# Kernel optimization log

Measured on AMD Instinct MI355X. Metric: run time of the kernel, lower is better.

The kernel has to match this reference:

```python
import jax, jax.numpy as jnp
import numpy as np

EMBED_DIM = 2048
NUM_Q_HEADS = 16
NUM_KV_HEADS = 4
HEAD_DIM = EMBED_DIM // NUM_Q_HEADS  # 128
N_REP = NUM_Q_HEADS // NUM_KV_HEADS  # 4


def setup_inputs() -> dict:
    key = jax.random.key(0)
    ks = jax.random.split(key, 8)
    B, T, C = 2, 2048, EMBED_DIM
    s = 0.02
    return {
        "x": jax.random.normal(ks[0], (B, T, C), dtype=jnp.float32),
        "Wq": jax.random.normal(ks[1], (C, NUM_Q_HEADS * HEAD_DIM), dtype=jnp.float32) * s,
        "bq": jax.random.normal(ks[2], (NUM_Q_HEADS * HEAD_DIM,), dtype=jnp.float32) * s,
        "Wk": jax.random.normal(ks[3], (C, NUM_KV_HEADS * HEAD_DIM), dtype=jnp.float32) * s,
        "bk": jax.random.normal(ks[4], (NUM_KV_HEADS * HEAD_DIM,), dtype=jnp.float32) * s,
        "Wv": jax.random.normal(ks[5], (C, NUM_KV_HEADS * HEAD_DIM), dtype=jnp.float32) * s,
        "bv": jax.random.normal(ks[6], (NUM_KV_HEADS * HEAD_DIM,), dtype=jnp.float32) * s,
        "Wo": jax.random.normal(ks[7], (C, C), dtype=jnp.float32) * s,
    }


def reference(x, Wq, bq, Wk, bk, Wv, bv, Wo):
    B, T, C = x.shape
    # Projections (torch Linear with bias; weights stored as [in, out])
    q = (x @ Wq + bq).reshape(B, T, NUM_KV_HEADS, N_REP, HEAD_DIM)
    k = (x @ Wk + bk).reshape(B, T, NUM_KV_HEADS, HEAD_DIM)
    v = (x @ Wv + bv).reshape(B, T, NUM_KV_HEADS, HEAD_DIM)
    # GQA: group query heads per kv head instead of materializing repeated K/V.
    # q: [B, G, n_rep, Tq, d], k/v: [B, G, Tk, d]
    q = q.transpose(0, 2, 3, 1, 4)  # B, G, n_rep, T, d
    k = k.transpose(0, 2, 1, 3)     # B, G, T, d
    v = v.transpose(0, 2, 1, 3)
    scale = 1.0 / jnp.sqrt(jnp.asarray(HEAD_DIM, dtype=x.dtype))
    scores = jnp.einsum('bgnqd,bgkd->bgnqk', q, k) * scale
    attn = jax.nn.softmax(scores, axis=-1)
    out = jnp.einsum('bgnqk,bgkd->bgnqd', attn, v)  # B, G, n_rep, T, d
    # merge heads back: (G, n_rep) -> Hq, then [B, T, C]
    out = out.transpose(0, 3, 1, 2, 4).reshape(B, T, C)
    return out @ Wo
```

## Files before the change

kernel.cpp:

```cpp
#include <hip/hip_runtime.h>
#include <hip/hip_bf16.h>
#include <cstdint>
#include <cstddef>

typedef __bf16 bf16;
typedef __attribute__((ext_vector_type(8))) __bf16 bf16x8;
typedef __attribute__((ext_vector_type(4))) float f32x4;
typedef __attribute__((ext_vector_type(16))) float f32x16;

#define KPAD 136

__device__ __forceinline__ void async16(const void* g, void* l) {
  __builtin_amdgcn_global_load_lds(
      (const __attribute__((address_space(1))) void*)g,
      (__attribute__((address_space(3))) void*)l,
      16, 0, 0);
}

__global__ void cvt_x(const float* __restrict__ in, bf16* __restrict__ out, int n8) {
  int i = blockIdx.x * 256 + threadIdx.x;
  if (i >= n8) return;
  const float* src = in + (size_t)i * 8;
  float4 f0 = *reinterpret_cast<const float4*>(src);
  float4 f1 = *reinterpret_cast<const float4*>(src + 4);
  bf16x8 v = {(bf16)f0.x, (bf16)f0.y, (bf16)f0.z, (bf16)f0.w,
              (bf16)f1.x, (bf16)f1.y, (bf16)f1.z, (bf16)f1.w};
  *reinterpret_cast<bf16x8*>(out + (size_t)i * 8) = v;
}

template <typename CT, bool HAS_BIAS>
__global__ __launch_bounds__(256, 2)
void gemm_bt(const bf16* __restrict__ A, const bf16* __restrict__ Bt,
             const bf16* __restrict__ bias, CT* __restrict__ C,
             int M, int N, int K) {
  __shared__ bf16 smem[4][128 * 64];
  const int tid = threadIdx.x;
  const int wave = tid >> 6, lane = tid & 63;
  const int quad = lane >> 4, l15 = lane & 15;
  const int row0 = blockIdx.y * 128;
  const int col0 = blockIdx.x * 128;
  const int wm = wave & 1, wn = wave >> 1;
  const int sw = l15 & 7;

  const f32x4 fz = {0.f, 0.f, 0.f, 0.f};
  f32x4 acc[4][4];
#pragma unroll
  for (int i = 0; i < 4; ++i)
#pragma unroll
    for (int j = 0; j < 4; ++j) acc[i][j] = fz;

#define STAGE(buf, k0)                                                         \
  {                                                                            \
    _Pragma("unroll")                                                          \
    for (int j = 0; j < 4; ++j) {                                              \
      int c = tid + j * 256;                                                   \
      int r = c >> 3;                                                          \
      int gs = (c & 7) ^ (r & 7);                                              \
      async16(A + (size_t)(row0 + r) * K + (k0) + gs * 8, &smem[(buf)*2][c * 8]);   \
      async16(Bt + (size_t)(col0 + r) * K + (k0) + gs * 8, &smem[(buf)*2 + 1][c * 8]); \
    }                                                                          \
  }

  STAGE(0, 0);
  __syncthreads();

  const int nt = K >> 6;
  for (int t = 0; t < nt; ++t) {
    const int cur = t & 1;
    if (t + 1 < nt) STAGE(cur ^ 1, (t + 1) << 6);

    const bf16* As = smem[cur * 2];
    const bf16* Bs = smem[cur * 2 + 1];
    bf16x8 a[4][2], b[4][2];
#pragma unroll
    for (int mf = 0; mf < 4; ++mf) {
      int ra = wm * 64 + mf * 16 + l15;
      int rb = wn * 64 + mf * 16 + l15;
#pragma unroll
      for (int ks = 0; ks < 2; ++ks) {
        int pg = (ks * 4 + quad) ^ sw;
        a[mf][ks] = *reinterpret_cast<const bf16x8*>(&As[ra * 64 + pg * 8]);
        b[mf][ks] = *reinterpret_cast<const bf16x8*>(&Bs[rb * 64 + pg * 8]);
      }
    }
#pragma unroll
    for (int ks = 0; ks < 2; ++ks)
#pragma unroll
      for (int mf = 0; mf < 4; ++mf)
#pragma unroll
        for (int nf = 0; nf < 4; ++nf)
          acc[mf][nf] = __builtin_amdgcn_mfma_f32_16x16x32_bf16(a[mf][ks], b[nf][ks],
                                                                acc[mf][nf], 0, 0, 0);

    __syncthreads();
  }
#undef STAGE

#pragma unroll
  for (int i = 0; i < 4; ++i) {
    int m = row0 + wm * 64 + i * 16 + quad * 4;
#pragma unroll
    for (int j = 0; j < 4; ++j) {
      int n = col0 + wn * 64 + j * 16 + l15;
      float bv = HAS_BIAS ? (float)bias[n] : 0.f;
#pragma unroll
      for (int r = 0; r < 4; ++r)
        C[(size_t)(m + r) * N + n] = (CT)(acc[i][j][r] + bv);
    }
  }
}

__global__ void transpose2d_cvt(const float* __restrict__ in, bf16* __restrict__ out,
                                int R, int C) {
  __shared__ float t[32][33];
  const int tx = threadIdx.x & 31, ty = threadIdx.x >> 5;
  const int c0 = blockIdx.x * 32, r0 = blockIdx.y * 32;
#pragma unroll
  for (int i = 0; i < 4; ++i)
    t[ty + i * 8][tx] = in[(size_t)(r0 + ty + i * 8) * C + c0 + tx];
  __syncthreads();
#pragma unroll
  for (int i = 0; i < 4; ++i)
    out[(size_t)(c0 + ty + i * 8) * R + r0 + tx] = (bf16)t[tx][ty + i * 8];
}

__global__ void transpose_v(const bf16* __restrict__ QKV, bf16* __restrict__ Vt) {
  const int z = blockIdx.z;
  const int b = z >> 2, g = z & 3;
  const bf16* in = QKV + (size_t)b * 2048 * 3072 + 2560 + g * 128;
  bf16* out = Vt + (size_t)z * 128 * 2048;
  __shared__ bf16 t[32][33];
  const int tx = threadIdx.x & 31, ty = threadIdx.x >> 5;
  const int d0 = blockIdx.x * 32;
  const int t0 = blockIdx.y * 32;
#pragma unroll
  for (int i = 0; i < 4; ++i)
    t[ty + i * 8][tx] = in[(size_t)(t0 + ty + i * 8) * 3072 + d0 + tx];
  __syncthreads();
#pragma unroll
  for (int i = 0; i < 4; ++i)
    out[(size_t)(d0 + ty + i * 8) * 2048 + t0 + tx] = t[tx][ty + i * 8];
}

__global__ void concat_bias(const float* __restrict__ bq, const float* __restrict__ bk,
                            const float* __restrict__ bv, bf16* __restrict__ out) {
  int i = blockIdx.x * 256 + threadIdx.x;
  float v;
  if (i < 2048) v = bq[i];
  else if (i < 2560) v = bk[i - 2048];
  else v = bv[i - 2560];
  out[i] = (bf16)v;
}

__global__ __launch_bounds__(256, 2)
void attn_kernel(const bf16* __restrict__ QKV, const bf16* __restrict__ Vt,
                 bf16* __restrict__ Out) {
  const int bid = blockIdx.x;
  const int qt = bid & 15;
  const int bh = bid >> 4;
  const int b = bh >> 4, h = bh & 15, g = h >> 2;
  const int tid = threadIdx.x;
  const int wave = tid >> 6, lane = tid & 63;
  const int l31 = lane & 31, half = lane >> 5;

  __shared__ bf16 smem[32768];
  bf16* Qstage = smem;

  const bf16* Qbase = QKV + ((size_t)b * 2048 + qt * 128) * 3072 + h * 128;
#pragma unroll
  for (int j = 0; j < 8; ++j) {
    int c = tid + j * 256;
    *reinterpret_cast<bf16x8*>(&Qstage[(c >> 4) * KPAD + (c & 15) * 8]) =
        *reinterpret_cast<const bf16x8*>(Qbase + (size_t)(c >> 4) * 3072 + (c & 15) * 8);
  }
  __syncthreads();
  bf16x8 qf[8];
#pragma unroll
  for (int ks = 0; ks < 8; ++ks)
    qf[ks] = *reinterpret_cast<const bf16x8*>(
        &Qstage[(wave * 32 + l31) * KPAD + ks * 16 + half * 8]);
  __syncthreads();

  const bf16* Kbase = QKV + (size_t)b * 2048 * 3072 + 2048 + g * 128;
  const bf16* Vbase = Vt + (size_t)(b * 4 + g) * 128 * 2048;

#define ATTN_STAGE(buf, t0_)                                                  \
  {                                                                           \
    bf16* KsD = smem + (buf)*16384;                                           \
    bf16* VsD = smem + (buf)*16384 + 8192;                                    \
    _Pragma("unroll")                                                         \
    for (int j = 0; j < 4; ++j) {                                             \
      int c = tid + j * 256;                                                  \
      int rk = c >> 4, gk = (c & 15) ^ (rk & 15);                             \
      async16(Kbase + (size_t)((t0_) + rk) * 3072 + gk * 8, &KsD[c * 8]);     \
      int rv = c >> 3, gv = (c & 7) ^ (rv & 7);                               \
      async16(Vbase + (size_t)rv * 2048 + (t0_) + gv * 8, &VsD[c * 8]);       \
    }                                                                         \
  }

  ATTN_STAGE(0, 0);
  __syncthreads();

  f32x16 po[4];
#pragma unroll
  for (int j = 0; j < 4; ++j)
#pragma unroll
    for (int r = 0; r < 16; ++r) po[j][r] = 0.f;
  float lsum = 0.f;
  const float sc2 = 0.12751746030545063f;

  for (int t = 0; t < 32; ++t) {
    const int cur = t & 1;
    if (t + 1 < 32) ATTN_STAGE(cur ^ 1, (t + 1) * 64);

    const bf16* KsB = smem + cur * 16384;
    const bf16* VsB = smem + cur * 16384 + 8192;

    f32x16 s[2];
#pragma unroll
    for (int nt = 0; nt < 2; ++nt)
#pragma unroll
      for (int r = 0; r < 16; ++r) s[nt][r] = 0.f;
#pragma unroll
    for (int ks = 0; ks < 8; ++ks) {
#pragma unroll
      for (int nt = 0; nt < 2; ++nt) {
        bf16x8 kf = *reinterpret_cast<const bf16x8*>(
            &KsB[(nt * 32 + l31) * 128 + (((ks * 2 + half) ^ (l31 & 15))) * 8]);
        s[nt] = __builtin_amdgcn_mfma_f32_32x32x16_bf16(kf, qf[ks], s[nt], 0, 0, 0);
      }
    }

#pragma unroll
    for (int nt = 0; nt < 2; ++nt)
#pragma unroll
      for (int r = 0; r < 16; ++r) {
        float p = exp2f(s[nt][r] * sc2);
        lsum += p;
        s[nt][r] = p;
      }

#pragma unroll
    for (int ks2 = 0; ks2 < 4; ++ks2) {
      const int nt = ks2 >> 1;
      const int a = (ks2 & 1) * 8;
      uint32_t x0, x1, x2, x3;
      asm("v_cvt_pk_bf16_f32 %0, %1, %2" : "=v"(x0) : "v"(s[nt][a + 0]), "v"(s[nt][a + 1]));
      asm("v_cvt_pk_bf16_f32 %0, %1, %2" : "=v"(x1) : "v"(s[nt][a + 2]), "v"(s[nt][a + 3]));
      asm("v_cvt_pk_bf16_f32 %0, %1, %2" : "=v"(x2) : "v"(s[nt][a + 4]), "v"(s[nt][a + 5]));
      asm("v_cvt_pk_bf16_f32 %0, %1, %2" : "=v"(x3) : "v"(s[nt][a + 6]), "v"(s[nt][a + 7]));
      asm("v_permlane32_swap_b32 %0, %1" : "+v"(x0), "+v"(x2));
      asm("v_permlane32_swap_b32 %0, %1" : "+v"(x1), "+v"(x3));
      union { uint32_t u[4]; bf16x8 v; } pu;
      pu.u[0] = x0; pu.u[1] = x1; pu.u[2] = x2; pu.u[3] = x3;
      const bf16x8 pf = pu.v;
#pragma unroll
      for (int nd = 0; nd < 4; ++nd) {
        bf16x8 vf = *reinterpret_cast<const bf16x8*>(
            &VsB[(nd * 32 + l31) * 64 + (((ks2 * 2 + half) ^ (l31 & 7))) * 8]);
        po[nd] = __builtin_amdgcn_mfma_f32_32x32x16_bf16(pf, vf, po[nd], 0, 0, 0);
      }
    }

    __syncthreads();
  }
#undef ATTN_STAGE

  float l = lsum + __shfl_xor(lsum, 32, 64);
  float inv = 1.0f / l;

  const size_t qrow0 = (size_t)b * 2048 + (size_t)qt * 128 + wave * 32;
#pragma unroll
  for (int r = 0; r < 16; ++r) {
    int row = (r & 3) + 8 * (r >> 2) + 4 * half;
    float invr = __shfl(inv, row, 64);
#pragma unroll
    for (int nt = 0; nt < 4; ++nt)
      Out[(qrow0 + row) * 2048 + h * 128 + nt * 32 + l31] = (bf16)(po[nt][r] * invr);
  }
}

extern "C" void kernel_launch(void* const* d_in, const int* in_sizes, int n_in,
                              void* d_out, int out_size, void* d_ws, size_t ws_size,
                              hipStream_t stream) {
  const float* x  = (const float*)d_in[0];
  const float* Wq = (const float*)d_in[1];
  const float* bq = (const float*)d_in[2];
  const float* Wk = (const float*)d_in[3];
  const float* bk = (const float*)d_in[4];
  const float* Wv = (const float*)d_in[5];
  const float* bv = (const float*)d_in[6];
  const float* Wo = (const float*)d_in[7];
  float* out = (float*)d_out;
  bf16* ws = (bf16*)d_ws;

  bf16* wqkvT = ws;
  bf16* biasq = ws + 6291456;
  bf16* woT   = ws + 6294528;
  bf16* qkv   = ws + 10488832;
  bf16* vt    = ws + 23071744;
  bf16* aout  = ws + 25168896;
  bf16* xb    = ws + 33557504;

  cvt_x<<<4096, 256, 0, stream>>>(x, xb, 1048576);
  transpose2d_cvt<<<dim3(64, 64), 256, 0, stream>>>(Wq, wqkvT, 2048, 2048);
  transpose2d_cvt<<<dim3(16, 64), 256, 0, stream>>>(Wk, wqkvT + 2048 * 2048, 2048, 512);
  transpose2d_cvt<<<dim3(16, 64), 256, 0, stream>>>(Wv, wqkvT + 2560 * 2048, 2048, 512);
  transpose2d_cvt<<<dim3(64, 64), 256, 0, stream>>>(Wo, woT, 2048, 2048);
  concat_bias<<<12, 256, 0, stream>>>(bq, bk, bv, biasq);

  gemm_bt<bf16, true><<<dim3(24, 32), 256, 0, stream>>>(xb, wqkvT, biasq, qkv, 4096, 3072, 2048);

  transpose_v<<<dim3(4, 64, 8), 256, 0, stream>>>(qkv, vt);

  attn_kernel<<<512, 256, 0, stream>>>(qkv, vt, aout);

  gemm_bt<float, false><<<dim3(16, 32), 256, 0, stream>>>(aout, woT, nullptr, out, 4096, 2048, 2048);
}
```

Before: 300.0 us.

## Register-staged K/V prefetch with padded LDS and XCD-aware GEMM tile swizzle

The attention kernel no longer uses direct global-to-LDS async loads with an XOR swizzle. Each K/V tile is now loaded into registers two iterations ahead and written into padded LDS rows (pitch 136 and 72) one iteration ahead, which removes the swizzle address math and deepens the prefetch. Separately, the GEMM remaps its block index so that consecutive tiles are grouped per XCD, aiming for better L2 locality. The cost is more VGPRs for the staging registers, a little more LDS, and extra VALU/LDS-store instructions in the loop.

```diff
diff --git a/kernel.cpp b/kernel.cpp
--- a/kernel.cpp
+++ b/kernel.cpp
@@ -9,6 +9,7 @@
 typedef __attribute__((ext_vector_type(16))) float f32x16;
 
 #define KPAD 136
+#define VPAD 72
 
 __device__ __forceinline__ void async16(const void* g, void* l) {
   __builtin_amdgcn_global_load_lds(
@@ -37,8 +38,16 @@
   const int tid = threadIdx.x;
   const int wave = tid >> 6, lane = tid & 63;
   const int quad = lane >> 4, l15 = lane & 15;
-  const int row0 = blockIdx.y * 128;
-  const int col0 = blockIdx.x * 128;
+
+  const int gx = gridDim.x;
+  const int nwg = gx * gridDim.y;
+  const int f = blockIdx.y * gx + blockIdx.x;
+  const int q8 = nwg >> 3, r8 = nwg & 7;
+  const int xcd = f & 7, idx = f >> 3;
+  const int swz = (xcd < r8 ? xcd * (q8 + 1) : r8 * (q8 + 1) + (xcd - r8) * q8) + idx;
+  const int row0 = (swz / gx) * 128;
+  const int col0 = (swz % gx) * 128;
+
   const int wm = wave & 1, wn = wave >> 1;
   const int sw = l15 & 7;
 
@@ -163,8 +172,35 @@
   const int wave = tid >> 6, lane = tid & 63;
   const int l31 = lane & 31, half = lane >> 5;
 
-  __shared__ bf16 smem[32768];
+  __shared__ bf16 smem[35840];
   bf16* Qstage = smem;
+
+  const bf16* Kbase = QKV + (size_t)b * 2048 * 3072 + 2048 + g * 128;
+  const bf16* Vbase = Vt + (size_t)(b * 4 + g) * 128 * 2048;
+
+  bf16x8 kreg[4], vreg[4];
+#define LOADT(t0_)                                                            \
+  {                                                                           \
+    _Pragma("unroll")                                                         \
+    for (int j = 0; j < 4; ++j) {                                             \
+      int c = tid + j * 256;                                                  \
+      kreg[j] = *reinterpret_cast<const bf16x8*>(                             \
+          Kbase + (size_t)((t0_) + (c >> 4)) * 3072 + (c & 15) * 8);          \
+      vreg[j] = *reinterpret_cast<const bf16x8*>(                             \
+          Vbase + (size_t)(c >> 3) * 2048 + (t0_) + (c & 7) * 8);             \
+    }                                                                         \
+  }
+#define WRITET(buf)                                                           \
+  {                                                                           \
+    bf16* KsD = smem + (buf)*17920;                                           \
+    bf16* VsD = KsD + 8704;                                                   \
+    _Pragma("unroll")                                                         \
+    for (int j = 0; j < 4; ++j) {                                             \
+      int c = tid + j * 256;                                                  \
+      *reinterpret_cast<bf16x8*>(&KsD[(c >> 4) * KPAD + (c & 15) * 8]) = kreg[j]; \
+      *reinterpret_cast<bf16x8*>(&VsD[(c >> 3) * VPAD + (c & 7) * 8]) = vreg[j]; \
+    }                                                                         \
+  }
 
   const bf16* Qbase = QKV + ((size_t)b * 2048 + qt * 128) * 3072 + h * 128;
 #pragma unroll
@@ -173,6 +209,7 @@
     *reinterpret_cast<bf16x8*>(&Qstage[(c >> 4) * KPAD + (c & 15) * 8]) =
         *reinterpret_cast<const bf16x8*>(Qbase + (size_t)(c >> 4) * 3072 + (c & 15) * 8);
   }
+  LOADT(0);
   __syncthreads();
   bf16x8 qf[8];
 #pragma unroll
@@ -181,24 +218,8 @@
         &Qstage[(wave * 32 + l31) * KPAD + ks * 16 + half * 8]);
   __syncthreads();
 
-  const bf16* Kbase = QKV + (size_t)b * 2048 * 3072 + 2048 + g * 128;
-  const bf16* Vbase = Vt + (size_t)(b * 4 + g) * 128 * 2048;
-
-#define ATTN_STAGE(buf, t0_)                                                  \
-  {                                                                           \
-    bf16* KsD = smem + (buf)*16384;                                           \
-    bf16* VsD = smem + (buf)*16384 + 8192;                                    \
-    _Pragma("unroll")                                                         \
-    for (int j = 0; j < 4; ++j) {                                             \
-      int c = tid + j * 256;                                                  \
-      int rk = c >> 4, gk = (c & 15) ^ (rk & 15);                             \
-      async16(Kbase + (size_t)((t0_) + rk) * 3072 + gk * 8, &KsD[c * 8]);     \
-      int rv = c >> 3, gv = (c & 7) ^ (rv & 7);                               \
-      async16(Vbase + (size_t)rv * 2048 + (t0_) + gv * 8, &VsD[c * 8]);       \
-    }                                                                         \
-  }
-
-  ATTN_STAGE(0, 0);
+  WRITET(0);
+  LOADT(64);
   __syncthreads();
 
   f32x16 po[4];
@@ -211,10 +232,11 @@
 
   for (int t = 0; t < 32; ++t) {
     const int cur = t & 1;
-    if (t + 1 < 32) ATTN_STAGE(cur ^ 1, (t + 1) * 64);
-
-    const bf16* KsB = smem + cur * 16384;
-    const bf16* VsB = smem + cur * 16384 + 8192;
+    const bf16* KsB = smem + cur * 17920;
+    const bf16* VsB = KsB + 8704;
+
+    if (t + 1 < 32) WRITET(cur ^ 1);
+    if (t + 2 < 32) LOADT((t + 2) * 64);
 
     f32x16 s[2];
 #pragma unroll
@@ -226,7 +248,7 @@
 #pragma unroll
       for (int nt = 0; nt < 2; ++nt) {
         bf16x8 kf = *reinterpret_cast<const bf16x8*>(
-            &KsB[(nt * 32 + l31) * 128 + (((ks * 2 + half) ^ (l31 & 15))) * 8]);
+            &KsB[(nt * 32 + l31) * KPAD + ks * 16 + half * 8]);
         s[nt] = __builtin_amdgcn_mfma_f32_32x32x16_bf16(kf, qf[ks], s[nt], 0, 0, 0);
       }
     }
@@ -257,14 +279,15 @@
 #pragma unroll
       for (int nd = 0; nd < 4; ++nd) {
         bf16x8 vf = *reinterpret_cast<const bf16x8*>(
-            &VsB[(nd * 32 + l31) * 64 + (((ks2 * 2 + half) ^ (l31 & 7))) * 8]);
+            &VsB[(nd * 32 + l31) * VPAD + ks2 * 16 + half * 8]);
         po[nd] = __builtin_amdgcn_mfma_f32_32x32x16_bf16(pf, vf, po[nd], 0, 0, 0);
       }
     }
 
     __syncthreads();
   }
-#undef ATTN_STAGE
+#undef LOADT
+#undef WRITET
 
   float l = lsum + __shfl_xor(lsum, 32, 64);
   float inv = 1.0f / l;
```

New measurement: 326.0 us. +8.7%, slower.
